# Optimization experiments

Hardware: AMD Instinct MI355X
Metric: run time of the kernel (lower is better)

## Reference

```python
import jax, jax.numpy as jnp
import numpy as np

B, N0, N1, FD, L, H = 4, 256, 256, 128, 3, 1
NG = N0 + N1            # nodes per graph
N = B * NG              # total nodes
EPS_BN = 1e-5
EPS_SM = 1e-16


def _build_edges():
    def perm_edges(n, off):
        idx = np.arange(n)
        a = np.repeat(idx, n); b = np.tile(idx, n)
        m = a != b
        return np.stack([a[m], b[m]]) + off
    e_intra = np.concatenate([perm_edges(N0, 0), perm_edges(N1, N0)], axis=1)
    a = np.arange(N0); b = np.arange(N0, N0 + N1)
    cross1 = np.stack([np.repeat(a, N1), np.tile(b, N0)])
    cross2 = np.stack([np.repeat(b, N0), np.tile(a, N1)])
    eg = np.concatenate([e_intra, cross1, cross2], axis=1)
    tg = np.concatenate([np.zeros(e_intra.shape[1], np.int32),
                         np.ones(cross1.shape[1] + cross2.shape[1], np.int32)])
    ei = np.concatenate([eg + g * NG for g in range(B)], axis=1).astype(np.int32)
    et = np.tile(tg, B).astype(np.int32)
    return jnp.asarray(ei), jnp.asarray(et)


def setup_inputs() -> dict:
    key = jax.random.key(0)
    ks = jax.random.split(key, 8)
    edge_index, edge_type = _build_edges()
    return {
        'desc0': jax.random.normal(ks[0], (B, FD, N0), jnp.float32),
        'desc1': jax.random.normal(ks[1], (B, FD, N1), jnp.float32),
        'W': jax.random.normal(ks[2], (L, 2, FD, H * FD), jnp.float32) * (1.0 / np.sqrt(FD)),
        'q': jax.random.normal(ks[3], (L, H * FD, H), jnp.float32) * 0.1,
        'k': jax.random.normal(ks[4], (L, H * FD, H), jnp.float32) * 0.1,
        'conv_b': jnp.zeros((L, FD), jnp.float32),
        'lin_W': jax.random.normal(ks[5], (L, FD, 2 * FD), jnp.float32) * (1.0 / np.sqrt(2 * FD)),
        'lin_b': jnp.zeros((L, FD), jnp.float32),
        'gamma': jnp.ones((L, FD), jnp.float32),
        'beta': jnp.zeros((L, FD), jnp.float32),
        'edge_index': edge_index,
        'edge_type': edge_type,
    }


def _forward(desc0, desc1, W, q, k, conv_b, lin_W, lin_b, gamma, beta, edge_index, edge_type):
    # x: [B, NG, FD] -> flattened batch graph [N, FD]
    x = jnp.concatenate([desc0, desc1], axis=2)        # [B, FD, NG]
    x = jnp.transpose(x, (0, 2, 1)).reshape(N, FD)
    src, dst = edge_index[0], edge_index[1]
    nlayers = W.shape[0]
    heads = q.shape[2]
    for l in range(nlayers):
        # relation-specific node projections (equiv to per-edge bmm with weight[edge_type])
        proj = jnp.einsum('nf,rfo->nro', x, W[l])       # [N, 2, H*FD]
        out_i = proj[dst, edge_type]                    # [E, H*FD]
        out_j = proj[src, edge_type]                    # [E, H*FD]
        alpha = jax.nn.leaky_relu(out_i @ q[l] + out_j @ k[l], 0.2)  # [E, H]
        # softmax over incoming edges of each destination node (across-relation)
        amax = jax.ops.segment_max(alpha, dst, num_segments=N)
        ex = jnp.exp(alpha - amax[dst])
        denom = jax.ops.segment_sum(ex, dst, num_segments=N)
        att = ex / (denom[dst] + EPS_SM)                # [E, H]
        msg = (att[:, :, None] * out_j.reshape(-1, heads, FD)).reshape(-1, heads * FD)
        agg = jax.ops.segment_sum(msg, dst, num_segments=N).reshape(N, heads, FD)
        m1 = jax.nn.relu(agg.mean(axis=1) + conv_b[l])  # concat=False -> mean over heads
        m2 = jnp.concatenate([x, m1], axis=1) @ lin_W[l].T + lin_b[l]
        mu = m2.mean(axis=0)
        var = ((m2 - mu) ** 2).mean(axis=0)             # biased var (BatchNorm training)
        m3 = (m2 - mu) / jnp.sqrt(var + EPS_BN) * gamma[l] + beta[l]
        x = x + m3
    x = x.reshape(B, NG, FD).transpose(0, 2, 1)         # [B, FD, NG]
    return x


def reference(desc0, desc1, W, q, k, conv_b, lin_W, lin_b, gamma, beta, edge_index, edge_type):
    x = _forward(desc0, desc1, W, q, k, conv_b, lin_W, lin_b, gamma, beta, edge_index, edge_type)
    return x[:, :, :N0], x[:, :, N0:]
```

## Files before the change

### kernel.cpp

```cpp
#include <hip/hip_runtime.h>

#define FD  128
#define NN  2048

#define OFF_X     0
#define OFF_PROJ  262144
#define OFF_QS    786432
#define OFF_KS    790528
#define OFF_M2    794624
#define OFF_SUMS  1056768
#define OFF_LWT   1057536

__device__ __forceinline__ void proj_qsks(
    const float* __restrict__ W, const float* __restrict__ qv,
    const float* __restrict__ kv, float* __restrict__ ws,
    int l, int n0, int t, const float (*xs)[FD],
    float (*redp)[256], float* red)
{
    int kh = t >> 8, tp = t & 255;
    int rsel = tp >> 7, o = tp & 127;
    const float* Wl = W + ((size_t)(l*2 + rsel)*FD)*FD + o;
    float acc[4] = {0.f, 0.f, 0.f, 0.f};
    int kbase = kh * 64;
    for (int k4 = kbase; k4 < kbase + 64; k4 += 4) {
        float w0 = Wl[(k4+0)*FD], w1 = Wl[(k4+1)*FD];
        float w2 = Wl[(k4+2)*FD], w3 = Wl[(k4+3)*FD];
#pragma unroll
        for (int r = 0; r < 4; r++) {
            float4 xq = *(const float4*)&xs[r][k4];
            acc[r] += xq.x*w0 + xq.y*w1 + xq.z*w2 + xq.w*w3;
        }
    }
    if (kh == 1) {
#pragma unroll
        for (int r = 0; r < 4; r++) redp[r][tp] = acc[r];
    }
    __syncthreads();
    if (t < 256) {
#pragma unroll
        for (int r = 0; r < 4; r++) acc[r] += redp[r][tp];
#pragma unroll
        for (int r = 0; r < 4; r++)
            ws[OFF_PROJ + (size_t)(n0 + r)*256 + tp] = acc[r];

        float qq = qv[l*FD + o], kq = kv[l*FD + o];
        int lane = t & 63, w = t >> 6;
#pragma unroll
        for (int r = 0; r < 4; r++) {
            float vq = acc[r]*qq, vk = acc[r]*kq;
            for (int off = 32; off; off >>= 1) {
                vq += __shfl_xor(vq, off, 64);
                vk += __shfl_xor(vk, off, 64);
            }
            if (lane == 0) { red[w*8 + r*2] = vq; red[w*8 + r*2 + 1] = vk; }
        }
    }
    __syncthreads();
    if (t < 16) {
        int r = t & 3, rs = (t >> 2) & 1, wh = t >> 3;
        float v = red[(rs*2)*8 + r*2 + wh] + red[(rs*2 + 1)*8 + r*2 + wh];
        if (wh == 0) ws[OFF_QS + rs*NN + n0 + r] = v;
        else         ws[OFF_KS + rs*NN + n0 + r] = v;
    }
}

__global__ __launch_bounds__(512, 4) void k_pre(
    const float* __restrict__ d0, const float* __restrict__ d1,
    const float* __restrict__ W,  const float* __restrict__ qv,
    const float* __restrict__ kv, const float* __restrict__ linW,
    float* __restrict__ ws)
{
    int bid = blockIdx.x, t = threadIdx.x;
    if (bid >= 512) {
        if (bid < 536) {
            int vb = bid - 512;
#pragma unroll
            for (int i = 0; i < 8; i++) {
                int e = vb*4096 + i*512 + t;
                int l = e >> 15, rem = e & 32767;
                int o = rem >> 8, c = rem & 255;
                ws[OFF_LWT + l*32768 + c*FD + o] = linW[e];
            }
        } else {
            for (int i = t; i < 768; i += 512) ws[OFF_SUMS + i] = 0.f;
        }
        return;
    }
    __shared__ __attribute__((aligned(16))) float xs[4][FD];
    __shared__ float redp[4][256];
    __shared__ float red[32];
    int n0 = bid * 4;
    {
        int row = t >> 7, f = t & 127;
        int n = n0 + row, gg = n >> 9, ii = n & 511;
        float v = (ii < 256) ? d0[gg*32768 + f*256 + ii]
                             : d1[gg*32768 + f*256 + (ii - 256)];
        xs[row][f] = v;
        ws[OFF_X + (size_t)n*FD + f] = v;
    }
    __syncthreads();
    proj_qsks(W, qv, kv, ws, 0, n0, t, xs, redp, red);
}

__global__ __launch_bounds__(512, 4) void k_bp(
    const float* __restrict__ W,     const float* __restrict__ qv,
    const float* __restrict__ kv,    const float* __restrict__ gamma,
    const float* __restrict__ beta,  float* __restrict__ ws, int l)
{
    __shared__ float scale[FD], shift[FD];
    __shared__ __attribute__((aligned(16))) float xs[4][FD];
    __shared__ float redp[4][256];
    __shared__ float red[32];
    int bid = blockIdx.x, t = threadIdx.x;
    int lp = l - 1;
    if (t < FD) {
        float mu  = ws[OFF_SUMS + lp*256 + t] * (1.f/2048.f);
        float var = ws[OFF_SUMS + lp*256 + 128 + t] * (1.f/2048.f) - mu*mu;
        float rs  = rsqrtf(var + 1e-5f);
        float gm  = gamma[lp*FD + t], bt = beta[lp*FD + t];
        scale[t] = gm * rs;
        shift[t] = bt - mu * gm * rs;
    }
    __syncthreads();
    int n0 = bid * 4;
    {
        int row = t >> 7, f = t & 127;
        size_t e = (size_t)(n0 + row)*FD + f;
        float xv = ws[OFF_X + e] + ws[OFF_M2 + e]*scale[f] + shift[f];
        xs[row][f] = xv;
        ws[OFF_X + e] = xv;
    }
    __syncthreads();
    proj_qsks(W, qv, kv, ws, l, n0, t, xs, redp, red);
}

__global__ __launch_bounds__(512, 4) void k_attn(
    const float* __restrict__ convb, const float* __restrict__ linb,
    float* __restrict__ ws, int l)
{
    __shared__ __attribute__((aligned(16))) float att[4*512];
    __shared__ __attribute__((aligned(16))) float redB[16*4*128];
    __shared__ __attribute__((aligned(16))) float cat[4*256];
    __shared__ float r1[FD], r2[FD];

    int bid = blockIdx.x, t = threadIdx.x;
    int dstbase = bid * 4;
    int g = dstbase >> 9, dloc0 = dstbase & 511;
    int Gd = (dloc0 >= 256) ? 1 : 0;

    if (t < 256) {
        int d = t >> 6, p = t & 63;
        int dloc = dloc0 + d;
        float q0 = ws[OFF_QS + dstbase + d];
        float q1 = ws[OFF_QS + NN + dstbase + d];
        float sc[8];
#pragma unroll
        for (int j = 0; j < 8; j++) {
            int s = p + j*64;
            int ts = (s < 256) ? Gd : 1 - Gd;
            float a = (ts ? q1 : q0) + ws[OFF_KS + ts*NN + g*512 + s];
            a = a > 0.f ? a : 0.2f*a;
            sc[j] = (s == dloc) ? -1e30f : a;
        }
        float lm = sc[0];
#pragma unroll
        for (int j = 1; j < 8; j++) lm = fmaxf(lm, sc[j]);
        for (int off = 32; off; off >>= 1) lm = fmaxf(lm, __shfl_xor(lm, off, 64));
        float ex[8], lsum = 0.f;
#pragma unroll
        for (int j = 0; j < 8; j++) { ex[j] = __expf(sc[j] - lm); lsum += ex[j]; }
        for (int off = 32; off; off >>= 1) lsum += __shfl_xor(lsum, off, 64);
        float inv = 1.f / (lsum + 1e-16f);
#pragma unroll
        for (int j = 0; j < 8; j++) att[d*512 + p + j*64] = ex[j]*inv;
    } else if (t < 384) {
        r1[t - 256] = 0.f;
    } else {
        r2[t - 384] = 0.f;
    }
    __syncthreads();

    int f4 = t & 31, sq = t >> 5;
    {
        int ts = (sq < 8) ? Gd : 1 - Gd;
        const float* P = ws + OFF_PROJ + (size_t)(g*512)*256 + ts*128 + f4*4;
        float acc[4][4];
#pragma unroll
        for (int d2 = 0; d2 < 4; d2++)
#pragma unroll
            for (int j = 0; j < 4; j++) acc[d2][j] = 0.f;
        int s0 = sq * 32;
#pragma unroll 4
        for (int i = 0; i < 32; i++) {
            int s = s0 + i;
            float4 p4 = *(const float4*)&P[(size_t)s*256];
            float b0 = att[0*512 + s], b1 = att[1*512 + s];
            float b2 = att[2*512 + s], b3 = att[3*512 + s];
            acc[0][0] += b0*p4.x; acc[0][1] += b0*p4.y; acc[0][2] += b0*p4.z; acc[0][3] += b0*p4.w;
            acc[1][0] += b1*p4.x; acc[1][1] += b1*p4.y; acc[1][2] += b1*p4.z; acc[1][3] += b1*p4.w;
            acc[2][0] += b2*p4.x; acc[2][1] += b2*p4.y; acc[2][2] += b2*p4.z; acc[2][3] += b2*p4.w;
            acc[3][0] += b3*p4.x; acc[3][1] += b3*p4.y; acc[3][2] += b3*p4.z; acc[3][3] += b3*p4.w;
        }
#pragma unroll
        for (int d2 = 0; d2 < 4; d2++)
            *(float4*)&redB[(sq*4 + d2)*128 + f4*4] =
                make_float4(acc[d2][0], acc[d2][1], acc[d2][2], acc[d2][3]);
    }
    __syncthreads();

    {
        int d2 = t >> 7, f = t & 127;
        float agg = 0.f;
#pragma unroll
        for (int sqi = 0; sqi < 16; sqi++) agg += redB[(sqi*4 + d2)*128 + f];
        float m1v = fmaxf(agg + convb[l*FD + f], 0.f);
        cat[d2*256 + FD + f] = m1v;
        cat[d2*256 + f] = ws[OFF_X + (size_t)(dstbase + d2)*FD + f];
    }
    __syncthreads();

    {
        const float* lwt = ws + OFF_LWT + l*32768 + f4*4;
        float mac[4][4];
#pragma unroll
        for (int d2 = 0; d2 < 4; d2++)
#pragma unroll
            for (int j = 0; j < 4; j++) mac[d2][j] = 0.f;
        int c0 = sq * 16;
#pragma unroll 4
        for (int i = 0; i < 16; i++) {
            int c = c0 + i;
            float4 w4 = *(const float4*)&lwt[c*128];
            float c0v = cat[0*256 + c], c1v = cat[1*256 + c];
            float c2v = cat[2*256 + c], c3v = cat[3*256 + c];
            mac[0][0] += c0v*w4.x; mac[0][1] += c0v*w4.y; mac[0][2] += c0v*w4.z; mac[0][3] += c0v*w4.w;
            mac[1][0] += c1v*w4.x; mac[1][1] += c1v*w4.y; mac[1][2] += c1v*w4.z; mac[1][3] += c1v*w4.w;
            mac[2][0] += c2v*w4.x; mac[2][1] += c2v*w4.y; mac[2][2] += c2v*w4.z; mac[2][3] += c2v*w4.w;
            mac[3][0] += c3v*w4.x; mac[3][1] += c3v*w4.y; mac[3][2] += c3v*w4.z; mac[3][3] += c3v*w4.w;
        }
#pragma unroll
        for (int d2 = 0; d2 < 4; d2++)
            *(float4*)&redB[(sq*4 + d2)*128 + f4*4] =
                make_float4(mac[d2][0], mac[d2][1], mac[d2][2], mac[d2][3]);
    }
    __syncthreads();

    {
        int d2 = t >> 7, o = t & 127;
        float m2v = linb[l*FD + o];
#pragma unroll
        for (int sqi = 0; sqi < 16; sqi++) m2v += redB[(sqi*4 + d2)*128 + o];
        ws[OFF_M2 + (size_t)(dstbase + d2)*FD + o] = m2v;
        atomicAdd(&r1[o], m2v);
        atomicAdd(&r2[o], m2v*m2v);
    }
    __syncthreads();
    if (t < 128) {
        atomicAdd(&ws[OFF_SUMS + l*256 + t],       r1[t]);
        atomicAdd(&ws[OFF_SUMS + l*256 + 128 + t], r2[t]);
    }
}

__global__ __launch_bounds__(256) void k_bnout(
    const float* __restrict__ gamma, const float* __restrict__ beta,
    float* __restrict__ ws, float* __restrict__ out)
{
    __shared__ float scale[FD], shift[FD];
    int bid = blockIdx.x, t = threadIdx.x;
    if (t < FD) {
        float mu  = ws[OFF_SUMS + 2*256 + t] * (1.f/2048.f);
        float var = ws[OFF_SUMS + 2*256 + 128 + t] * (1.f/2048.f) - mu*mu;
        float rs  = rsqrtf(var + 1e-5f);
        float gm  = gamma[2*FD + t], bt = beta[2*FD + t];
        scale[t] = gm * rs;
        shift[t] = bt - mu * gm * rs;
    }
    __syncthreads();
#pragma unroll
    for (int i = 0; i < 2; i++) {
        int idx = bid*512 + i*256 + t;
        int f = idx & 127, n = idx >> 7;
        float v = ws[OFF_X + idx] + ws[OFF_M2 + idx]*scale[f] + shift[f];
        int gg = n >> 9, ii = n & 511;
        int off = (ii < 256) ? (gg*32768 + f*256 + ii)
                             : (131072 + gg*32768 + f*256 + (ii - 256));
        out[off] = v;
    }
}

extern "C" void kernel_launch(void* const* d_in, const int* in_sizes, int n_in,
                              void* d_out, int out_size, void* d_ws, size_t ws_size,
                              hipStream_t stream) {
    (void)in_sizes; (void)n_in; (void)out_size; (void)ws_size;
    const float* desc0 = (const float*)d_in[0];
    const float* desc1 = (const float*)d_in[1];
    const float* W     = (const float*)d_in[2];
    const float* q     = (const float*)d_in[3];
    const float* kk    = (const float*)d_in[4];
    const float* convb = (const float*)d_in[5];
    const float* linW  = (const float*)d_in[6];
    const float* linb  = (const float*)d_in[7];
    const float* gamma = (const float*)d_in[8];
    const float* beta  = (const float*)d_in[9];
    float* ws  = (float*)d_ws;
    float* out = (float*)d_out;

    hipLaunchKernelGGL(k_pre,  dim3(537), dim3(512), 0, stream, desc0, desc1, W, q, kk, linW, ws);
    hipLaunchKernelGGL(k_attn, dim3(512), dim3(512), 0, stream, convb, linb, ws, 0);
    hipLaunchKernelGGL(k_bp,   dim3(512), dim3(512), 0, stream, W, q, kk, gamma, beta, ws, 1);
    hipLaunchKernelGGL(k_attn, dim3(512), dim3(512), 0, stream, convb, linb, ws, 1);
    hipLaunchKernelGGL(k_bp,   dim3(512), dim3(512), 0, stream, W, q, kk, gamma, beta, ws, 2);
    hipLaunchKernelGGL(k_attn, dim3(512), dim3(512), 0, stream, convb, linb, ws, 2);
    hipLaunchKernelGGL(k_bnout, dim3(512), dim3(256), 0, stream, gamma, beta, ws, out);
}
```

Before: 186.6 us.

## Aggregate raw features before projection and fold q/k into W-vectors

Stops materialising the per-node relation projections (x@W). Attention logits now use precomputed W·q and W·k vectors, so each node needs only a dot product. The attention kernel first aggregates raw x rows with the attention weights per relation group, then applies W to the aggregated vectors, which reassociates the matmul. Block-to-node mapping is swizzled and the occupancy hint is lowered. This trades a large projection pass and its workspace traffic for a small extra matmul per destination block, plus more shared-memory reduction stages.

```diff
diff --git a/kernel.cpp b/kernel.cpp
--- a/kernel.cpp
+++ b/kernel.cpp
@@ -1,70 +1,46 @@
 #include <hip/hip_runtime.h>
 
-#define FD  128
-#define NN  2048
+#define FD 128
+#define NN 2048
 
 #define OFF_X     0
-#define OFF_PROJ  262144
-#define OFF_QS    786432
-#define OFF_KS    790528
-#define OFF_M2    794624
-#define OFF_SUMS  1056768
-#define OFF_LWT   1057536
-
-__device__ __forceinline__ void proj_qsks(
-    const float* __restrict__ W, const float* __restrict__ qv,
-    const float* __restrict__ kv, float* __restrict__ ws,
-    int l, int n0, int t, const float (*xs)[FD],
-    float (*redp)[256], float* red)
-{
-    int kh = t >> 8, tp = t & 255;
-    int rsel = tp >> 7, o = tp & 127;
-    const float* Wl = W + ((size_t)(l*2 + rsel)*FD)*FD + o;
-    float acc[4] = {0.f, 0.f, 0.f, 0.f};
-    int kbase = kh * 64;
-    for (int k4 = kbase; k4 < kbase + 64; k4 += 4) {
-        float w0 = Wl[(k4+0)*FD], w1 = Wl[(k4+1)*FD];
-        float w2 = Wl[(k4+2)*FD], w3 = Wl[(k4+3)*FD];
-#pragma unroll
-        for (int r = 0; r < 4; r++) {
-            float4 xq = *(const float4*)&xs[r][k4];
-            acc[r] += xq.x*w0 + xq.y*w1 + xq.z*w2 + xq.w*w3;
-        }
-    }
-    if (kh == 1) {
-#pragma unroll
-        for (int r = 0; r < 4; r++) redp[r][tp] = acc[r];
-    }
-    __syncthreads();
-    if (t < 256) {
-#pragma unroll
-        for (int r = 0; r < 4; r++) acc[r] += redp[r][tp];
-#pragma unroll
-        for (int r = 0; r < 4; r++)
-            ws[OFF_PROJ + (size_t)(n0 + r)*256 + tp] = acc[r];
-
-        float qq = qv[l*FD + o], kq = kv[l*FD + o];
-        int lane = t & 63, w = t >> 6;
-#pragma unroll
-        for (int r = 0; r < 4; r++) {
-            float vq = acc[r]*qq, vk = acc[r]*kq;
-            for (int off = 32; off; off >>= 1) {
-                vq += __shfl_xor(vq, off, 64);
-                vk += __shfl_xor(vk, off, 64);
-            }
-            if (lane == 0) { red[w*8 + r*2] = vq; red[w*8 + r*2 + 1] = vk; }
-        }
-    }
-    __syncthreads();
-    if (t < 16) {
-        int r = t & 3, rs = (t >> 2) & 1, wh = t >> 3;
-        float v = red[(rs*2)*8 + r*2 + wh] + red[(rs*2 + 1)*8 + r*2 + wh];
-        if (wh == 0) ws[OFF_QS + rs*NN + n0 + r] = v;
-        else         ws[OFF_KS + rs*NN + n0 + r] = v;
-    }
-}
-
-__global__ __launch_bounds__(512, 4) void k_pre(
+#define OFF_M2    262144
+#define OFF_QS    524288
+#define OFF_KS    528384
+#define OFF_SUMS  532480
+#define OFF_LWT   533248
+#define OFF_WQ    631552
+#define OFF_WK    632320
+
+__device__ __forceinline__ int swizzle_n0(int bid) {
+    int g    = (bid & 7) >> 1;
+    int slot = ((bid >> 3) << 1) | (bid & 1);
+    return g*512 + slot*4;
+}
+
+__device__ __forceinline__ void qsks4(
+    const float* __restrict__ wqp, const float* __restrict__ wkp,
+    float* __restrict__ ws, int n0, int t, const float (*xs)[FD])
+{
+    int did = t >> 5, f4 = t & 31;
+    int row = did >> 2, r = (did >> 1) & 1, isK = did & 1;
+    const float* vec = (isK ? wkp : wqp) + r*FD;
+    float4 x4 = *(const float4*)&xs[row][f4*4];
+    float4 v4 = *(const float4*)&vec[f4*4];
+    float a = x4.x*v4.x + x4.y*v4.y + x4.z*v4.z + x4.w*v4.w;
+    a += __shfl_xor(a, 16, 64);
+    a += __shfl_xor(a, 8, 64);
+    a += __shfl_xor(a, 4, 64);
+    a += __shfl_xor(a, 2, 64);
+    a += __shfl_xor(a, 1, 64);
+    if ((t & 31) == 0) {
+        int n = n0 + row;
+        if (isK) ws[OFF_KS + r*NN + n] = a;
+        else     ws[OFF_QS + r*NN + n] = a;
+    }
+}
+
+__global__ __launch_bounds__(512) void k_pre(
     const float* __restrict__ d0, const float* __restrict__ d1,
     const float* __restrict__ W,  const float* __restrict__ qv,
     const float* __restrict__ kv, const float* __restrict__ linW,
@@ -81,15 +57,43 @@
                 int o = rem >> 8, c = rem & 255;
                 ws[OFF_LWT + l*32768 + c*FD + o] = linW[e];
             }
+        } else if (bid < 542) {
+            int vb = bid - 536;
+            int l = vb >> 1, r = vb & 1;
+            if (t < 128) {
+                const float* Wr = W + ((size_t)((l*2 + r)*FD + t))*FD;
+                float aq = 0.f, ak = 0.f;
+                for (int o = 0; o < FD; o += 4) {
+                    float4 w4 = *(const float4*)&Wr[o];
+                    float4 q4 = *(const float4*)&qv[l*FD + o];
+                    float4 k4 = *(const float4*)&kv[l*FD + o];
+                    aq += w4.x*q4.x + w4.y*q4.y + w4.z*q4.z + w4.w*q4.w;
+                    ak += w4.x*k4.x + w4.y*k4.y + w4.z*k4.z + w4.w*k4.w;
+                }
+                ws[OFF_WQ + (l*2 + r)*FD + t] = aq;
+                ws[OFF_WK + (l*2 + r)*FD + t] = ak;
+            }
         } else {
             for (int i = t; i < 768; i += 512) ws[OFF_SUMS + i] = 0.f;
         }
         return;
     }
+    __shared__ __attribute__((aligned(16))) float wqk[4][FD];
     __shared__ __attribute__((aligned(16))) float xs[4][FD];
-    __shared__ float redp[4][256];
-    __shared__ float red[32];
-    int n0 = bid * 4;
+    {
+        int pair = t & 255, which = t >> 8;
+        int r = pair >> 7, f = pair & 127;
+        const float* Wr = W + ((size_t)(r*FD + f))*FD;
+        const float* v  = which ? kv : qv;
+        float a = 0.f;
+        for (int o = 0; o < FD; o += 4) {
+            float4 w4 = *(const float4*)&Wr[o];
+            float4 v4 = *(const float4*)&v[o];
+            a += w4.x*v4.x + w4.y*v4.y + w4.z*v4.z + w4.w*v4.w;
+        }
+        wqk[which*2 + r][f] = a;
+    }
+    int n0 = swizzle_n0(bid);
     {
         int row = t >> 7, f = t & 127;
         int n = n0 + row, gg = n >> 9, ii = n & 511;
@@ -99,21 +103,18 @@
         ws[OFF_X + (size_t)n*FD + f] = v;
     }
     __syncthreads();
-    proj_qsks(W, qv, kv, ws, 0, n0, t, xs, redp, red);
-}
-
-__global__ __launch_bounds__(512, 4) void k_bp(
-    const float* __restrict__ W,     const float* __restrict__ qv,
-    const float* __restrict__ kv,    const float* __restrict__ gamma,
-    const float* __restrict__ beta,  float* __restrict__ ws, int l)
+    qsks4(&wqk[0][0], &wqk[2][0], ws, n0, t, xs);
+}
+
+__global__ __launch_bounds__(512) void k_bp(
+    const float* __restrict__ gamma, const float* __restrict__ beta,
+    float* __restrict__ ws, int l)
 {
     __shared__ float scale[FD], shift[FD];
     __shared__ __attribute__((aligned(16))) float xs[4][FD];
-    __shared__ float redp[4][256];
-    __shared__ float red[32];
     int bid = blockIdx.x, t = threadIdx.x;
     int lp = l - 1;
-    if (t < FD) {
+    if (t < 128) {
         float mu  = ws[OFF_SUMS + lp*256 + t] * (1.f/2048.f);
         float var = ws[OFF_SUMS + lp*256 + 128 + t] * (1.f/2048.f) - mu*mu;
         float rs  = rsqrtf(var + 1e-5f);
@@ -122,37 +123,38 @@
         shift[t] = bt - mu * gm * rs;
     }
     __syncthreads();
-    int n0 = bid * 4;
+    int n0 = swizzle_n0(bid);
     {
         int row = t >> 7, f = t & 127;
         size_t e = (size_t)(n0 + row)*FD + f;
         float xv = ws[OFF_X + e] + ws[OFF_M2 + e]*scale[f] + shift[f];
+        ws[OFF_X + e] = xv;
         xs[row][f] = xv;
-        ws[OFF_X + e] = xv;
-    }
-    __syncthreads();
-    proj_qsks(W, qv, kv, ws, l, n0, t, xs, redp, red);
-}
-
-__global__ __launch_bounds__(512, 4) void k_attn(
-    const float* __restrict__ convb, const float* __restrict__ linb,
-    float* __restrict__ ws, int l)
+    }
+    __syncthreads();
+    qsks4(ws + OFF_WQ + l*2*FD, ws + OFF_WK + l*2*FD, ws, n0, t, xs);
+}
+
+__global__ __launch_bounds__(512, 2) void k_attn(
+    const float* __restrict__ W,     const float* __restrict__ convb,
+    const float* __restrict__ linb,  float* __restrict__ ws, int l)
 {
     __shared__ __attribute__((aligned(16))) float att[4*512];
-    __shared__ __attribute__((aligned(16))) float redB[16*4*128];
+    __shared__ __attribute__((aligned(16))) float redB[4*512];
+    __shared__ __attribute__((aligned(16))) float yb[2*4*128];
     __shared__ __attribute__((aligned(16))) float cat[4*256];
     __shared__ float r1[FD], r2[FD];
 
     int bid = blockIdx.x, t = threadIdx.x;
-    int dstbase = bid * 4;
-    int g = dstbase >> 9, dloc0 = dstbase & 511;
+    int n0 = swizzle_n0(bid);
+    int g = n0 >> 9, dloc0 = n0 & 511;
     int Gd = (dloc0 >= 256) ? 1 : 0;
 
     if (t < 256) {
         int d = t >> 6, p = t & 63;
         int dloc = dloc0 + d;
-        float q0 = ws[OFF_QS + dstbase + d];
-        float q1 = ws[OFF_QS + NN + dstbase + d];
+        float q0 = ws[OFF_QS + n0 + d];
+        float q1 = ws[OFF_QS + NN + n0 + d];
         float sc[8];
 #pragma unroll
         for (int j = 0; j < 8; j++) {
@@ -180,77 +182,158 @@
     }
     __syncthreads();
 
-    int f4 = t & 31, sq = t >> 5;
-    {
-        int ts = (sq < 8) ? Gd : 1 - Gd;
-        const float* P = ws + OFF_PROJ + (size_t)(g*512)*256 + ts*128 + f4*4;
-        float acc[4][4];
-#pragma unroll
-        for (int d2 = 0; d2 < 4; d2++)
-#pragma unroll
-            for (int j = 0; j < 4; j++) acc[d2][j] = 0.f;
-        int s0 = sq * 32;
+    int f4 = t & 31, c = t >> 5, w = t >> 6, lane = t & 63;
+    float acc[4][4];
+
+#pragma unroll
+    for (int d2 = 0; d2 < 4; d2++)
+#pragma unroll
+        for (int j = 0; j < 4; j++) acc[d2][j] = 0.f;
+    {
+        const float* X = ws + OFF_X + (size_t)(g*512)*FD + f4*4;
+        int s0 = c*32;
 #pragma unroll 4
         for (int i = 0; i < 32; i++) {
             int s = s0 + i;
-            float4 p4 = *(const float4*)&P[(size_t)s*256];
-            float b0 = att[0*512 + s], b1 = att[1*512 + s];
-            float b2 = att[2*512 + s], b3 = att[3*512 + s];
-            acc[0][0] += b0*p4.x; acc[0][1] += b0*p4.y; acc[0][2] += b0*p4.z; acc[0][3] += b0*p4.w;
-            acc[1][0] += b1*p4.x; acc[1][1] += b1*p4.y; acc[1][2] += b1*p4.z; acc[1][3] += b1*p4.w;
-            acc[2][0] += b2*p4.x; acc[2][1] += b2*p4.y; acc[2][2] += b2*p4.z; acc[2][3] += b2*p4.w;
-            acc[3][0] += b3*p4.x; acc[3][1] += b3*p4.y; acc[3][2] += b3*p4.z; acc[3][3] += b3*p4.w;
-        }
-#pragma unroll
-        for (int d2 = 0; d2 < 4; d2++)
-            *(float4*)&redB[(sq*4 + d2)*128 + f4*4] =
-                make_float4(acc[d2][0], acc[d2][1], acc[d2][2], acc[d2][3]);
-    }
-    __syncthreads();
-
-    {
-        int d2 = t >> 7, f = t & 127;
-        float agg = 0.f;
-#pragma unroll
-        for (int sqi = 0; sqi < 16; sqi++) agg += redB[(sqi*4 + d2)*128 + f];
-        float m1v = fmaxf(agg + convb[l*FD + f], 0.f);
-        cat[d2*256 + FD + f] = m1v;
-        cat[d2*256 + f] = ws[OFF_X + (size_t)(dstbase + d2)*FD + f];
-    }
-    __syncthreads();
-
-    {
-        const float* lwt = ws + OFF_LWT + l*32768 + f4*4;
-        float mac[4][4];
-#pragma unroll
-        for (int d2 = 0; d2 < 4; d2++)
-#pragma unroll
-            for (int j = 0; j < 4; j++) mac[d2][j] = 0.f;
-        int c0 = sq * 16;
+            float4 x4 = *(const float4*)&X[(size_t)s*FD];
+#pragma unroll
+            for (int d2 = 0; d2 < 4; d2++) {
+                float b = att[d2*512 + s];
+                acc[d2][0] += b*x4.x; acc[d2][1] += b*x4.y;
+                acc[d2][2] += b*x4.z; acc[d2][3] += b*x4.w;
+            }
+        }
+    }
+#pragma unroll
+    for (int d2 = 0; d2 < 4; d2++)
+#pragma unroll
+        for (int j = 0; j < 4; j++) acc[d2][j] += __shfl_xor(acc[d2][j], 32, 64);
+    {
+        int h = w >> 2, chf = w & 3;
+        if (chf >= 2 && lane < 32) {
+            int slot = h*2 + chf - 2;
+#pragma unroll
+            for (int d2 = 0; d2 < 4; d2++)
+                *(float4*)&redB[slot*512 + d2*128 + f4*4] =
+                    make_float4(acc[d2][0], acc[d2][1], acc[d2][2], acc[d2][3]);
+        }
+        __syncthreads();
+        if (chf < 2 && lane < 32) {
+            int slot = h*2 + chf;
+#pragma unroll
+            for (int d2 = 0; d2 < 4; d2++) {
+                float4 p4 = *(const float4*)&redB[slot*512 + d2*128 + f4*4];
+                *(float4*)&redB[slot*512 + d2*128 + f4*4] =
+                    make_float4(acc[d2][0]+p4.x, acc[d2][1]+p4.y,
+                                acc[d2][2]+p4.z, acc[d2][3]+p4.w);
+            }
+        }
+        __syncthreads();
+#pragma unroll
+        for (int jj = 0; jj < 2; jj++) {
+            int idx = t + jj*512;
+            int hh = idx >> 9, rem = idx & 511;
+            yb[hh*512 + rem] = redB[(hh*2)*512 + rem] + redB[(hh*2 + 1)*512 + rem];
+        }
+        __syncthreads();
+    }
+
+#pragma unroll
+    for (int d2 = 0; d2 < 4; d2++)
+#pragma unroll
+        for (int j = 0; j < 4; j++) acc[d2][j] = 0.f;
+    {
+        int hA = c >> 3, fb = (c & 7)*16;
+        int rel = (hA == 0) ? Gd : 1 - Gd;
+        const float* Wm = W + ((size_t)((l*2 + rel)*FD + fb))*FD + f4*4;
 #pragma unroll 4
         for (int i = 0; i < 16; i++) {
-            int c = c0 + i;
-            float4 w4 = *(const float4*)&lwt[c*128];
-            float c0v = cat[0*256 + c], c1v = cat[1*256 + c];
-            float c2v = cat[2*256 + c], c3v = cat[3*256 + c];
-            mac[0][0] += c0v*w4.x; mac[0][1] += c0v*w4.y; mac[0][2] += c0v*w4.z; mac[0][3] += c0v*w4.w;
-            mac[1][0] += c1v*w4.x; mac[1][1] += c1v*w4.y; mac[1][2] += c1v*w4.z; mac[1][3] += c1v*w4.w;
-            mac[2][0] += c2v*w4.x; mac[2][1] += c2v*w4.y; mac[2][2] += c2v*w4.z; mac[2][3] += c2v*w4.w;
-            mac[3][0] += c3v*w4.x; mac[3][1] += c3v*w4.y; mac[3][2] += c3v*w4.z; mac[3][3] += c3v*w4.w;
-        }
+            float4 w4 = *(const float4*)&Wm[(size_t)i*FD];
+#pragma unroll
+            for (int d2 = 0; d2 < 4; d2++) {
+                float yv = yb[hA*512 + d2*128 + fb + i];
+                acc[d2][0] += yv*w4.x; acc[d2][1] += yv*w4.y;
+                acc[d2][2] += yv*w4.z; acc[d2][3] += yv*w4.w;
+            }
+        }
+    }
+#pragma unroll
+    for (int d2 = 0; d2 < 4; d2++)
+#pragma unroll
+        for (int j = 0; j < 4; j++) acc[d2][j] += __shfl_xor(acc[d2][j], 32, 64);
+    if (w >= 4 && lane < 32) {
 #pragma unroll
         for (int d2 = 0; d2 < 4; d2++)
-            *(float4*)&redB[(sq*4 + d2)*128 + f4*4] =
-                make_float4(mac[d2][0], mac[d2][1], mac[d2][2], mac[d2][3]);
-    }
-    __syncthreads();
-
-    {
-        int d2 = t >> 7, o = t & 127;
-        float m2v = linb[l*FD + o];
-#pragma unroll
-        for (int sqi = 0; sqi < 16; sqi++) m2v += redB[(sqi*4 + d2)*128 + o];
-        ws[OFF_M2 + (size_t)(dstbase + d2)*FD + o] = m2v;
+            *(float4*)&redB[(w-4)*512 + d2*128 + f4*4] =
+                make_float4(acc[d2][0], acc[d2][1], acc[d2][2], acc[d2][3]);
+    }
+    __syncthreads();
+    if (w < 4 && lane < 32) {
+#pragma unroll
+        for (int d2 = 0; d2 < 4; d2++) {
+            float4 p4 = *(const float4*)&redB[w*512 + d2*128 + f4*4];
+            *(float4*)&redB[w*512 + d2*128 + f4*4] =
+                make_float4(acc[d2][0]+p4.x, acc[d2][1]+p4.y,
+                            acc[d2][2]+p4.z, acc[d2][3]+p4.w);
+        }
+    }
+    __syncthreads();
+    {
+        int d = t >> 7, f = t & 127;
+        float aggv = redB[0*512 + d*128 + f] + redB[1*512 + d*128 + f]
+                   + redB[2*512 + d*128 + f] + redB[3*512 + d*128 + f];
+        float m1v = fmaxf(aggv + convb[l*FD + f], 0.f);
+        cat[d*256 + FD + f] = m1v;
+        cat[d*256 + f] = ws[OFF_X + (size_t)(n0 + d)*FD + f];
+    }
+    __syncthreads();
+
+#pragma unroll
+    for (int d2 = 0; d2 < 4; d2++)
+#pragma unroll
+        for (int j = 0; j < 4; j++) acc[d2][j] = 0.f;
+    {
+        const float* lwt = ws + OFF_LWT + l*32768 + f4*4;
+        int c0 = c*16;
+#pragma unroll 4
+        for (int i = 0; i < 16; i++) {
+            int cc = c0 + i;
+            float4 w4 = *(const float4*)&lwt[(size_t)cc*FD];
+#pragma unroll
+            for (int d2 = 0; d2 < 4; d2++) {
+                float cv = cat[d2*256 + cc];
+                acc[d2][0] += cv*w4.x; acc[d2][1] += cv*w4.y;
+                acc[d2][2] += cv*w4.z; acc[d2][3] += cv*w4.w;
+            }
+        }
+    }
+#pragma unroll
+    for (int d2 = 0; d2 < 4; d2++)
+#pragma unroll
+        for (int j = 0; j < 4; j++) acc[d2][j] += __shfl_xor(acc[d2][j], 32, 64);
+    if (w >= 4 && lane < 32) {
+#pragma unroll
+        for (int d2 = 0; d2 < 4; d2++)
+            *(float4*)&redB[(w-4)*512 + d2*128 + f4*4] =
+                make_float4(acc[d2][0], acc[d2][1], acc[d2][2], acc[d2][3]);
+    }
+    __syncthreads();
+    if (w < 4 && lane < 32) {
+#pragma unroll
+        for (int d2 = 0; d2 < 4; d2++) {
+            float4 p4 = *(const float4*)&redB[w*512 + d2*128 + f4*4];
+            *(float4*)&redB[w*512 + d2*128 + f4*4] =
+                make_float4(acc[d2][0]+p4.x, acc[d2][1]+p4.y,
+                            acc[d2][2]+p4.z, acc[d2][3]+p4.w);
+        }
+    }
+    __syncthreads();
+    {
+        int d = t >> 7, o = t & 127;
+        float m2v = linb[l*FD + o]
+                  + redB[0*512 + d*128 + o] + redB[1*512 + d*128 + o]
+                  + redB[2*512 + d*128 + o] + redB[3*512 + d*128 + o];
+        ws[OFF_M2 + (size_t)(n0 + d)*FD + o] = m2v;
         atomicAdd(&r1[o], m2v);
         atomicAdd(&r2[o], m2v*m2v);
     }
@@ -267,7 +350,7 @@
 {
     __shared__ float scale[FD], shift[FD];
     int bid = blockIdx.x, t = threadIdx.x;
-    if (t < FD) {
+    if (t < 128) {
         float mu  = ws[OFF_SUMS + 2*256 + t] * (1.f/2048.f);
         float var = ws[OFF_SUMS + 2*256 + 128 + t] * (1.f/2048.f) - mu*mu;
         float rs  = rsqrtf(var + 1e-5f);
@@ -305,11 +388,12 @@
     float* ws  = (float*)d_ws;
     float* out = (float*)d_out;
 
-    hipLaunchKernelGGL(k_pre,  dim3(537), dim3(512), 0, stream, desc0, desc1, W, q, kk, linW, ws);
-    hipLaunchKernelGGL(k_attn, dim3(512), dim3(512), 0, stream, convb, linb, ws, 0);
-    hipLaunchKernelGGL(k_bp,   dim3(512), dim3(512), 0, stream, W, q, kk, gamma, beta, ws, 1);
-    hipLaunchKernelGGL(k_attn, dim3(512), dim3(512), 0, stream, convb, linb, ws, 1);
-    hipLaunchKernelGGL(k_bp,   dim3(512), dim3(512), 0, stream, W, q, kk, gamma, beta, ws, 2);
-    hipLaunchKernelGGL(k_attn, dim3(512), dim3(512), 0, stream, convb, linb, ws, 2);
+    hipLaunchKernelGGL(k_pre,  dim3(543), dim3(512), 0, stream,
+                       desc0, desc1, W, q, kk, linW, ws);
+    hipLaunchKernelGGL(k_attn, dim3(512), dim3(512), 0, stream, W, convb, linb, ws, 0);
+    hipLaunchKernelGGL(k_bp,   dim3(512), dim3(512), 0, stream, gamma, beta, ws, 1);
+    hipLaunchKernelGGL(k_attn, dim3(512), dim3(512), 0, stream, W, convb, linb, ws, 1);
+    hipLaunchKernelGGL(k_bp,   dim3(512), dim3(512), 0, stream, gamma, beta, ws, 2);
+    hipLaunchKernelGGL(k_attn, dim3(512), dim3(512), 0, stream, W, convb, linb, ws, 2);
     hipLaunchKernelGGL(k_bnout, dim3(512), dim3(256), 0, stream, gamma, beta, ws, out);
 }
```

New measurement: 194.3 us. +4.1%, slower.
